# Kernel optimization log

Hardware: AMD Instinct MI355X
Metric: run time of the kernel (lower is better)

Reference implementation:

```python
import jax, jax.numpy as jnp
import numpy as np

D_MODEL = 1024  # scale uses sqrt(d_model), matching the source's sqrt(C)

def setup_inputs() -> dict:
    key = jax.random.key(0)
    kx, kq, kk, kv = jax.random.split(key, 4)
    B, T, C, H = 8, 2048, D_MODEL, 64
    s = 1.0 / np.sqrt(C)
    return {
        "x": jax.random.normal(kx, (B, T, C), dtype=jnp.float32),
        "Wq": jax.random.normal(kq, (C, H), dtype=jnp.float32) * s,
        "Wk": jax.random.normal(kk, (C, H), dtype=jnp.float32) * s,
        "Wv": jax.random.normal(kv, (C, H), dtype=jnp.float32) * s,
    }

def reference(x, Wq, Wk, Wv):
    B, T, C = x.shape
    q = jnp.einsum("btc,ch->bth", x, Wq)
    k = jnp.einsum("btc,ch->bth", x, Wk)
    v = jnp.einsum("btc,ch->bth", x, Wv)
    # scores scaled by 1/sqrt(C) (C = d_model), faithful to source
    wei = jnp.einsum("bth,bsh->bts", q, k) / jnp.sqrt(jnp.float32(C))
    causal = jnp.tril(jnp.ones((T, T), dtype=bool))  # [T, T]
    wei = jnp.where(causal, wei, -jnp.inf)
    wei = jax.nn.softmax(wei, axis=-1)
    out = jnp.einsum("bts,bsh->bth", wei, v)
    return out
```

## Files before the change

kernel.cpp:

```cpp
#include <hip/hip_runtime.h>

typedef unsigned short u16;
typedef __attribute__((ext_vector_type(4))) float f32x4;
typedef __attribute__((ext_vector_type(8))) short bf16x8;
typedef __attribute__((ext_vector_type(4))) u16 u16x4;
typedef __attribute__((ext_vector_type(8))) u16 u16x8;

#define MFMA(a, b, c) __builtin_amdgcn_mfma_f32_16x16x32_bf16(a, b, c, 0, 0, 0)

__device__ __forceinline__ u16 f2bf(float f) {
    unsigned u = __float_as_uint(f);
    u += 0x7fffu + ((u >> 16) & 1u);
    return (u16)(u >> 16);
}
__device__ __forceinline__ float bf2f(u16 h) {
    unsigned u = ((unsigned)h) << 16;
    return __uint_as_float(u);
}

__device__ __forceinline__ void load_lds16(const void* g, void* l) {
    __builtin_amdgcn_global_load_lds((const __attribute__((address_space(1))) void*)g,
                                     (__attribute__((address_space(3))) void*)l,
                                     16, 0, 0);
}

__global__ void wt_pack(const float* __restrict__ Wq, const float* __restrict__ Wk,
                        const float* __restrict__ Wv, u16* __restrict__ Wtt) {
    const int k = blockIdx.x;
    const int n = threadIdx.x;
    const float* W = (n < 64) ? Wq : (n < 128 ? Wk : Wv);
    const float v = W[(size_t)k * 64 + (n & 63)];
    const int kt = k >> 5, ks = k & 31, c = ks >> 3, ci = ks & 7;
    Wtt[(size_t)kt * 6144 + n * 32 + (((c ^ (n & 3)) << 3) + ci)] = f2bf(v);
}

__global__ __launch_bounds__(256, 4) void qkv_gemm(const float* __restrict__ x,
                                                   const u16* __restrict__ Wtt,
                                                   u16* __restrict__ qo,
                                                   u16* __restrict__ ko,
                                                   u16* __restrict__ vT) {
    const int tid = threadIdx.x;
    const int lane = tid & 63, wave = tid >> 6;
    const int lr = lane & 15, lg = lane >> 4;
    const int m0 = blockIdx.x * 32;

    __shared__ __align__(16) float xs[2][32 * 32];
    __shared__ __align__(16) u16 ws[2][192 * 32];

    f32x4 acc[2][3];
#pragma unroll
    for (int m = 0; m < 2; ++m)
#pragma unroll
        for (int n = 0; n < 3; ++n) acc[m][n] = (f32x4){0.f, 0.f, 0.f, 0.f};

    const int xrow = tid >> 3, xc = tid & 7;

#define QSTAGE(bufi, kt_)                                                              \
    {                                                                                  \
        load_lds16(x + (size_t)(m0 + xrow) * 1024 + (kt_)*32 + ((xc ^ (xrow & 7)) << 2), \
                   &xs[bufi][wave * 256]);                                             \
        _Pragma("unroll") for (int j = 0; j < 3; ++j) {                                \
            load_lds16(Wtt + (size_t)(kt_)*6144 + (j * 256 + tid) * 8,                 \
                       &ws[bufi][(j * 256 + wave * 64) * 8]);                          \
        }                                                                              \
    }

    QSTAGE(0, 0);
    __syncthreads();

    for (int kt = 0; kt < 32; ++kt) {
        const int cur = kt & 1;
        if (kt < 31) QSTAGE(cur ^ 1, kt + 1);

        bf16x8 a[2];
#pragma unroll
        for (int mm = 0; mm < 2; ++mm) {
            const int rr = mm * 16 + lr;
            const int g0 = lg * 2;
            f32x4 f0 = *(const f32x4*)&xs[cur][rr * 32 + ((g0 ^ (rr & 7)) << 2)];
            f32x4 f1 = *(const f32x4*)&xs[cur][rr * 32 + (((g0 + 1) ^ (rr & 7)) << 2)];
            bf16x8 t;
#pragma unroll
            for (int i = 0; i < 4; ++i) {
                t[i] = (short)f2bf(f0[i]);
                t[i + 4] = (short)f2bf(f1[i]);
            }
            a[mm] = t;
        }
#pragma unroll
        for (int nl = 0; nl < 3; ++nl) {
            const int row = (wave * 3 + nl) * 16 + lr;
            const bf16x8 b = *(const bf16x8*)&ws[cur][row * 32 + ((lg ^ (row & 3)) << 3)];
            acc[0][nl] = MFMA(a[0], b, acc[0][nl]);
            acc[1][nl] = MFMA(a[1], b, acc[1][nl]);
        }
        __syncthreads();
    }

    const float SCQ = 0.0450842200277801f;
    const int bb = m0 >> 11;
    const int tb = m0 & 2047;
#pragma unroll
    for (int mm = 0; mm < 2; ++mm)
#pragma unroll
        for (int nl = 0; nl < 3; ++nl) {
            const int col = (wave * 3 + nl) * 16 + lr;
            const int rl = mm * 16 + lg * 4;
            if (col < 64) {
#pragma unroll
                for (int r = 0; r < 4; ++r)
                    qo[(size_t)(m0 + rl + r) * 64 + col] = f2bf(acc[mm][nl][r] * SCQ);
            } else if (col < 128) {
#pragma unroll
                for (int r = 0; r < 4; ++r)
                    ko[(size_t)(m0 + rl + r) * 64 + (col - 64)] = f2bf(acc[mm][nl][r]);
            } else {
                u16x4 pk;
#pragma unroll
                for (int r = 0; r < 4; ++r) pk[r] = f2bf(acc[mm][nl][r]);
                *(u16x4*)&vT[(size_t)(bb * 64 + (col - 128)) * 2048 + tb + rl] = pk;
            }
        }
}

#define PPITCH 72
__global__ __launch_bounds__(256, 3) void attn_part(const u16* __restrict__ q,
                                                    const u16* __restrict__ k,
                                                    const u16* __restrict__ vT,
                                                    u16* __restrict__ Opb,
                                                    float* __restrict__ Lp) {
    const int b = blockIdx.x & 7;
    int g = blockIdx.x >> 3;
    int qt = 31, rem = g;
    while (rem >= (qt >> 3) + 1) { rem -= (qt >> 3) + 1; --qt; }
    const int c0 = rem;
    const int q0 = qt * 64;
    const int kv_lo = c0 * 512;
    const int kv_hi = min(kv_lo + 512, q0 + 64);
    const int ntiles = (kv_hi - kv_lo) >> 6;
    const int slot = (b * 32 + qt) * 4 + c0;

    __shared__ __align__(16) u16 lK[2][64 * 64];
    __shared__ __align__(16) u16 lV[2][64 * 64];
    __shared__ __align__(16) u16 lP[4][16 * PPITCH];

    const int tid = threadIdx.x;
    const int wave = tid >> 6, lane = tid & 63;
    const int lr = lane & 15, lg = lane >> 4;

    const u16* qb = q + (size_t)b * 2048 * 64;
    const u16* kb = k + (size_t)b * 2048 * 64;
    const u16* vb = vT + (size_t)b * 64 * 2048;

    const int myrow = q0 + wave * 16 + lr;
    const bf16x8 qf0 = *(const bf16x8*)(qb + (size_t)myrow * 64 + lg * 8);
    const bf16x8 qf1 = *(const bf16x8*)(qb + (size_t)myrow * 64 + 32 + lg * 8);

    f32x4 oacc[4];
#pragma unroll
    for (int n = 0; n < 4; ++n) oacc[n] = (f32x4){0.f, 0.f, 0.f, 0.f};
    float rs = 0.f;

#define ASTAGE(bufi, kv0_)                                                             \
    {                                                                                  \
        _Pragma("unroll") for (int j = 0; j < 2; ++j) {                                \
            const int cid = j * 256 + wave * 64 + lane;                                \
            const int row = cid >> 3, cc = cid & 7;                                    \
            load_lds16(kb + (size_t)((kv0_) + row) * 64 + ((cc ^ (row & 7)) << 3),     \
                       &lK[bufi][(j * 256 + wave * 64) * 8]);                          \
            load_lds16(vb + (size_t)row * 2048 + (kv0_) + ((cc ^ (row & 7)) << 3),     \
                       &lV[bufi][(j * 256 + wave * 64) * 8]);                          \
        }                                                                              \
    }

    ASTAGE(0, kv_lo);
    __syncthreads();

    for (int it = 0; it < ntiles; ++it) {
        const int cur = it & 1;
        if (it + 1 < ntiles) ASTAGE(cur ^ 1, kv_lo + (it + 1) * 64);

        const int kv0 = kv_lo + it * 64;
        if (kv0 <= q0 + wave * 16 + 15) {
            f32x4 s[4];
            __builtin_amdgcn_s_setprio(1);
#pragma unroll
            for (int n = 0; n < 4; ++n) {
                const int row = n * 16 + lr;
                const bf16x8 kf0 = *(const bf16x8*)&lK[cur][row * 64 + ((lg ^ (row & 7)) << 3)];
                const bf16x8 kf1 =
                    *(const bf16x8*)&lK[cur][row * 64 + (((4 + lg) ^ (row & 7)) << 3)];
                f32x4 a = (f32x4){0.f, 0.f, 0.f, 0.f};
                a = MFMA(kf0, qf0, a);
                a = MFMA(kf1, qf1, a);
                s[n] = a;
            }
            __builtin_amdgcn_s_setprio(0);

            const bool msk = (kv0 + 63 > q0 + wave * 16);
#pragma unroll
            for (int n = 0; n < 4; ++n) {
                u16x4 pk;
#pragma unroll
                for (int r = 0; r < 4; ++r) {
                    const int kvi = kv0 + n * 16 + lg * 4 + r;
                    const float p = (!msk || kvi <= myrow) ? exp2f(s[n][r]) : 0.f;
                    rs += p;
                    pk[r] = f2bf(p);
                }
                *(u16x4*)&lP[wave][lr * PPITCH + n * 16 + lg * 4] = pk;
            }

            __builtin_amdgcn_s_setprio(1);
#pragma unroll
            for (int kc = 0; kc < 2; ++kc) {
                const bf16x8 pf = *(const bf16x8*)&lP[wave][lr * PPITCH + kc * 32 + lg * 8];
#pragma unroll
                for (int n = 0; n < 4; ++n) {
                    const int row = n * 16 + lr;
                    const bf16x8 vf =
                        *(const bf16x8*)&lV[cur][row * 64 + (((kc * 4 + lg) ^ (row & 7)) << 3)];
                    oacc[n] = MFMA(pf, vf, oacc[n]);
                }
            }
            __builtin_amdgcn_s_setprio(0);
        }
        __syncthreads();
    }

    rs += __shfl_xor(rs, 16);
    rs += __shfl_xor(rs, 32);
    if (lane < 16) Lp[slot * 64 + wave * 16 + lr] = rs;

    u16* op = Opb + (size_t)slot * 4096 + wave * 1024;
#pragma unroll
    for (int n = 0; n < 4; ++n)
#pragma unroll
        for (int r = 0; r < 4; ++r)
            op[n * 256 + (lg * 4 + r) * 16 + lr] = f2bf(oacc[n][r]);
}

__global__ __launch_bounds__(256) void attn_combine(const u16* __restrict__ Opb,
                                                    const float* __restrict__ Lp,
                                                    float* __restrict__ out) {
    const int gid = blockIdx.x * 256 + threadIdx.x;
    const int colg = gid & 7;
    const int row = gid >> 3;
    const int b = row >> 11, tt = row & 2047;
    const int qt = tt >> 6, i = tt & 63;
    const int nc = (qt >> 3) + 1;
    const size_t sbase = (size_t)(b * 32 + qt) * 4;
    const int sub0 = (i >> 4) * 1024 + (colg >> 1) * 256 + (i & 15) * 16 + (colg & 1) * 8;

    float O[8] = {0.f, 0.f, 0.f, 0.f, 0.f, 0.f, 0.f, 0.f};
    float L = 0.f;
    for (int c = 0; c < nc; ++c) {
        const u16x8 v = *(const u16x8*)&Opb[(sbase + c) * 4096 + sub0];
#pragma unroll
        for (int j = 0; j < 8; ++j) O[j] += bf2f(v[j]);
        L += Lp[(sbase + c) * 64 + i];
    }
    const float rinv = 1.0f / L;
    f32x4 o0, o1;
#pragma unroll
    for (int j = 0; j < 4; ++j) {
        o0[j] = O[j] * rinv;
        o1[j] = O[4 + j] * rinv;
    }
    float* ob = out + (size_t)row * 64 + colg * 8;
    *(f32x4*)(ob) = o0;
    *(f32x4*)(ob + 4) = o1;
}

extern "C" void kernel_launch(void* const* d_in, const int* in_sizes, int n_in,
                              void* d_out, int out_size, void* d_ws, size_t ws_size,
                              hipStream_t stream) {
    const float* x = (const float*)d_in[0];
    const float* Wq = (const float*)d_in[1];
    const float* Wk = (const float*)d_in[2];
    const float* Wv = (const float*)d_in[3];
    float* out = (float*)d_out;

    char* ws = (char*)d_ws;
    u16* Wtt = (u16*)ws;
    u16* qb = (u16*)(ws + (512 << 10));
    u16* kb = (u16*)(ws + (512 << 10) + (2 << 20));
    u16* vT = (u16*)(ws + (512 << 10) + (4 << 20));
    u16* Opb = (u16*)(ws + (8 << 20));
    float* Lp = (float*)(ws + (20 << 20));

    wt_pack<<<1024, 192, 0, stream>>>(Wq, Wk, Wv, Wtt);
    qkv_gemm<<<512, 256, 0, stream>>>(x, Wtt, qb, kb, vT);
    attn_part<<<640, 256, 0, stream>>>(qb, kb, vT, Opb, Lp);
    attn_combine<<<512, 256, 0, stream>>>(Opb, Lp, out);
}
```

Measured before the change: 56.28 us.

## Retile QKV projection GEMM to 64x64 tiles split per matrix

The QKV projection GEMM moves from 32-row tiles covering all 192 output columns to 64-row by 64-column tiles, one matrix (Q, K or V) per block. The grid grows from 512 to 768 blocks, the K-step doubles to 64 so there are fewer loop iterations and barriers, and the weight packing layout and swizzle are rebuilt to match. Each block now reads 64 rows of fp32 x per stage but covers only one of three outputs, so x is read from global memory three times instead of once. The larger LDS footprint lowers the launch-bounds occupancy hint from 4 to 3.

```diff
diff --git a/kernel.cpp b/kernel.cpp
--- a/kernel.cpp
+++ b/kernel.cpp
@@ -30,11 +30,12 @@
     const int n = threadIdx.x;
     const float* W = (n < 64) ? Wq : (n < 128 ? Wk : Wv);
     const float v = W[(size_t)k * 64 + (n & 63)];
-    const int kt = k >> 5, ks = k & 31, c = ks >> 3, ci = ks & 7;
-    Wtt[(size_t)kt * 6144 + n * 32 + (((c ^ (n & 3)) << 3) + ci)] = f2bf(v);
-}
-
-__global__ __launch_bounds__(256, 4) void qkv_gemm(const float* __restrict__ x,
+    const int mat = n >> 6, nl = n & 63;
+    const int kt = k >> 6, ks = k & 63, c = ks >> 3, ci = ks & 7;
+    Wtt[(size_t)((mat * 16 + kt) * 64 + nl) * 64 + (((c ^ (nl & 7)) << 3) + ci)] = f2bf(v);
+}
+
+__global__ __launch_bounds__(256, 3) void qkv_gemm(const float* __restrict__ x,
                                                    const u16* __restrict__ Wtt,
                                                    u16* __restrict__ qo,
                                                    u16* __restrict__ ko,
@@ -42,85 +43,91 @@
     const int tid = threadIdx.x;
     const int lane = tid & 63, wave = tid >> 6;
     const int lr = lane & 15, lg = lane >> 4;
-    const int m0 = blockIdx.x * 32;
-
-    __shared__ __align__(16) float xs[2][32 * 32];
-    __shared__ __align__(16) u16 ws[2][192 * 32];
-
-    f32x4 acc[2][3];
-#pragma unroll
-    for (int m = 0; m < 2; ++m)
-#pragma unroll
-        for (int n = 0; n < 3; ++n) acc[m][n] = (f32x4){0.f, 0.f, 0.f, 0.f};
-
-    const int xrow = tid >> 3, xc = tid & 7;
-
-#define QSTAGE(bufi, kt_)                                                              \
-    {                                                                                  \
-        load_lds16(x + (size_t)(m0 + xrow) * 1024 + (kt_)*32 + ((xc ^ (xrow & 7)) << 2), \
-                   &xs[bufi][wave * 256]);                                             \
-        _Pragma("unroll") for (int j = 0; j < 3; ++j) {                                \
-            load_lds16(Wtt + (size_t)(kt_)*6144 + (j * 256 + tid) * 8,                 \
-                       &ws[bufi][(j * 256 + wave * 64) * 8]);                          \
-        }                                                                              \
+    const int mat = blockIdx.x >> 8;
+    const int m0 = (blockIdx.x & 255) * 64;
+
+    __shared__ __align__(16) float xs[2][64 * 64];
+    __shared__ __align__(16) u16 ws[2][64 * 64];
+
+    f32x4 acc[4];
+#pragma unroll
+    for (int m = 0; m < 4; ++m) acc[m] = (f32x4){0.f, 0.f, 0.f, 0.f};
+
+#define QSTAGE(bufi, kt_)                                                               \
+    {                                                                                   \
+        _Pragma("unroll") for (int j = 0; j < 4; ++j) {                                 \
+            const int cid = j * 256 + tid;                                              \
+            const int row = cid >> 4, cc = cid & 15;                                    \
+            load_lds16(x + (size_t)(m0 + row) * 1024 + (kt_)*64 +                       \
+                           ((cc ^ (row & 7)) << 2),                                     \
+                       &xs[bufi][(j * 256 + wave * 64) * 4]);                           \
+        }                                                                               \
+        _Pragma("unroll") for (int j = 0; j < 2; ++j) {                                 \
+            const int cid = j * 256 + tid;                                              \
+            load_lds16(Wtt + (size_t)(mat * 16 + (kt_)) * 4096 + cid * 8,               \
+                       &ws[bufi][(j * 256 + wave * 64) * 8]);                           \
+        }                                                                               \
     }
 
     QSTAGE(0, 0);
     __syncthreads();
 
-    for (int kt = 0; kt < 32; ++kt) {
+    for (int kt = 0; kt < 16; ++kt) {
         const int cur = kt & 1;
-        if (kt < 31) QSTAGE(cur ^ 1, kt + 1);
-
-        bf16x8 a[2];
-#pragma unroll
-        for (int mm = 0; mm < 2; ++mm) {
-            const int rr = mm * 16 + lr;
-            const int g0 = lg * 2;
-            f32x4 f0 = *(const f32x4*)&xs[cur][rr * 32 + ((g0 ^ (rr & 7)) << 2)];
-            f32x4 f1 = *(const f32x4*)&xs[cur][rr * 32 + (((g0 + 1) ^ (rr & 7)) << 2)];
-            bf16x8 t;
-#pragma unroll
-            for (int i = 0; i < 4; ++i) {
-                t[i] = (short)f2bf(f0[i]);
-                t[i + 4] = (short)f2bf(f1[i]);
+        if (kt < 15) QSTAGE(cur ^ 1, kt + 1);
+
+#pragma unroll
+        for (int h = 0; h < 2; ++h) {
+            const int wrow = wave * 16 + lr;
+            const int cb = h * 4 + lg;
+            const bf16x8 b = *(const bf16x8*)&ws[cur][wrow * 64 + ((cb ^ (wrow & 7)) << 3)];
+#pragma unroll
+            for (int mm = 0; mm < 4; ++mm) {
+                const int rr = mm * 16 + lr;
+                const int c0 = h * 8 + lg * 2;
+                f32x4 f0 = *(const f32x4*)&xs[cur][rr * 64 + ((c0 ^ (rr & 7)) << 2)];
+                f32x4 f1 = *(const f32x4*)&xs[cur][rr * 64 + (((c0 + 1) ^ (rr & 7)) << 2)];
+                bf16x8 a;
+#pragma unroll
+                for (int i = 0; i < 4; ++i) {
+                    a[i] = (short)f2bf(f0[i]);
+                    a[i + 4] = (short)f2bf(f1[i]);
+                }
+                acc[mm] = MFMA(a, b, acc[mm]);
             }
-            a[mm] = t;
-        }
-#pragma unroll
-        for (int nl = 0; nl < 3; ++nl) {
-            const int row = (wave * 3 + nl) * 16 + lr;
-            const bf16x8 b = *(const bf16x8*)&ws[cur][row * 32 + ((lg ^ (row & 3)) << 3)];
-            acc[0][nl] = MFMA(a[0], b, acc[0][nl]);
-            acc[1][nl] = MFMA(a[1], b, acc[1][nl]);
         }
         __syncthreads();
     }
 
     const float SCQ = 0.0450842200277801f;
-    const int bb = m0 >> 11;
-    const int tb = m0 & 2047;
-#pragma unroll
-    for (int mm = 0; mm < 2; ++mm)
-#pragma unroll
-        for (int nl = 0; nl < 3; ++nl) {
-            const int col = (wave * 3 + nl) * 16 + lr;
-            const int rl = mm * 16 + lg * 4;
-            if (col < 64) {
-#pragma unroll
-                for (int r = 0; r < 4; ++r)
-                    qo[(size_t)(m0 + rl + r) * 64 + col] = f2bf(acc[mm][nl][r] * SCQ);
-            } else if (col < 128) {
-#pragma unroll
-                for (int r = 0; r < 4; ++r)
-                    ko[(size_t)(m0 + rl + r) * 64 + (col - 64)] = f2bf(acc[mm][nl][r]);
-            } else {
-                u16x4 pk;
-#pragma unroll
-                for (int r = 0; r < 4; ++r) pk[r] = f2bf(acc[mm][nl][r]);
-                *(u16x4*)&vT[(size_t)(bb * 64 + (col - 128)) * 2048 + tb + rl] = pk;
-            }
-        }
+    const int col = wave * 16 + lr;
+    if (mat == 0) {
+#pragma unroll
+        for (int mm = 0; mm < 4; ++mm) {
+            const int rl = m0 + mm * 16 + lg * 4;
+#pragma unroll
+            for (int r = 0; r < 4; ++r)
+                qo[(size_t)(rl + r) * 64 + col] = f2bf(acc[mm][r] * SCQ);
+        }
+    } else if (mat == 1) {
+#pragma unroll
+        for (int mm = 0; mm < 4; ++mm) {
+            const int rl = m0 + mm * 16 + lg * 4;
+#pragma unroll
+            for (int r = 0; r < 4; ++r)
+                ko[(size_t)(rl + r) * 64 + col] = f2bf(acc[mm][r]);
+        }
+    } else {
+        const int bb = m0 >> 11;
+        const int tb = m0 & 2047;
+#pragma unroll
+        for (int mm = 0; mm < 4; ++mm) {
+            u16x4 pk;
+#pragma unroll
+            for (int r = 0; r < 4; ++r) pk[r] = f2bf(acc[mm][r]);
+            *(u16x4*)&vT[(size_t)(bb * 64 + col) * 2048 + tb + mm * 16 + lg * 4] = pk;
+        }
+    }
 }
 
 #define PPITCH 72
@@ -290,7 +297,7 @@
     float* Lp = (float*)(ws + (20 << 20));
 
     wt_pack<<<1024, 192, 0, stream>>>(Wq, Wk, Wv, Wtt);
-    qkv_gemm<<<512, 256, 0, stream>>>(x, Wtt, qb, kb, vT);
+    qkv_gemm<<<768, 256, 0, stream>>>(x, Wtt, qb, kb, vT);
     attn_part<<<640, 256, 0, stream>>>(qb, kb, vT, Opb, Lp);
     attn_combine<<<512, 256, 0, stream>>>(Opb, Lp, out);
 }
```

Result: slower. 60.42 us (+7.4%).

## Retile QKV projection GEMM to 64x96 block tiles with 2x2 wave grid

Applied to the files above, without the earlier changes.

Each QKV projection block now computes a 64-row by 96-column tile instead of 32 rows by all 192 columns. The K step grows from 32 to 64, and the four waves are arranged as a 2x2 grid. The weight pack layout changes to match: column-tile-major with an 8-way XOR swizzle. The aim is more MFMA work per LDS stage and fewer loop iterations and barriers. In exchange, each x row is now loaded and converted to bf16 by two blocks, and the larger LDS footprint lowers occupancy to two blocks per CU.

```diff
diff --git a/kernel.cpp b/kernel.cpp
--- a/kernel.cpp
+++ b/kernel.cpp
@@ -30,11 +30,12 @@
     const int n = threadIdx.x;
     const float* W = (n < 64) ? Wq : (n < 128 ? Wk : Wv);
     const float v = W[(size_t)k * 64 + (n & 63)];
-    const int kt = k >> 5, ks = k & 31, c = ks >> 3, ci = ks & 7;
-    Wtt[(size_t)kt * 6144 + n * 32 + (((c ^ (n & 3)) << 3) + ci)] = f2bf(v);
-}
-
-__global__ __launch_bounds__(256, 4) void qkv_gemm(const float* __restrict__ x,
+    const int nt = n / 96, nl = n % 96;
+    const int kt = k >> 6, ks = k & 63, c = ks >> 3, ci = ks & 7;
+    Wtt[(size_t)((nt * 16 + kt) * 96 + nl) * 64 + (((c ^ (nl & 7)) << 3) + ci)] = f2bf(v);
+}
+
+__global__ __launch_bounds__(256, 2) void qkv_gemm(const float* __restrict__ x,
                                                    const u16* __restrict__ Wtt,
                                                    u16* __restrict__ qo,
                                                    u16* __restrict__ ko,
@@ -42,10 +43,12 @@
     const int tid = threadIdx.x;
     const int lane = tid & 63, wave = tid >> 6;
     const int lr = lane & 15, lg = lane >> 4;
-    const int m0 = blockIdx.x * 32;
-
-    __shared__ __align__(16) float xs[2][32 * 32];
-    __shared__ __align__(16) u16 ws[2][192 * 32];
+    const int wr = wave >> 1, wc = wave & 1;
+    const int mt = blockIdx.x >> 1, nt = blockIdx.x & 1;
+    const int m0 = mt * 64;
+
+    __shared__ __align__(16) float xs[2][64 * 64];
+    __shared__ __align__(16) u16 ws[2][96 * 64];
 
     f32x4 acc[2][3];
 #pragma unroll
@@ -53,46 +56,54 @@
 #pragma unroll
         for (int n = 0; n < 3; ++n) acc[m][n] = (f32x4){0.f, 0.f, 0.f, 0.f};
 
-    const int xrow = tid >> 3, xc = tid & 7;
-
-#define QSTAGE(bufi, kt_)                                                              \
-    {                                                                                  \
-        load_lds16(x + (size_t)(m0 + xrow) * 1024 + (kt_)*32 + ((xc ^ (xrow & 7)) << 2), \
-                   &xs[bufi][wave * 256]);                                             \
-        _Pragma("unroll") for (int j = 0; j < 3; ++j) {                                \
-            load_lds16(Wtt + (size_t)(kt_)*6144 + (j * 256 + tid) * 8,                 \
-                       &ws[bufi][(j * 256 + wave * 64) * 8]);                          \
-        }                                                                              \
+#define QSTAGE(bufi, kt_)                                                               \
+    {                                                                                   \
+        _Pragma("unroll") for (int j = 0; j < 4; ++j) {                                 \
+            const int cid = j * 256 + tid;                                              \
+            const int row = cid >> 4, cc = cid & 15;                                    \
+            load_lds16(x + (size_t)(m0 + row) * 1024 + (kt_)*64 +                       \
+                           ((cc ^ (row & 7)) << 2),                                     \
+                       &xs[bufi][(j * 256 + wave * 64) * 4]);                           \
+        }                                                                               \
+        _Pragma("unroll") for (int j = 0; j < 3; ++j) {                                 \
+            const int cid = j * 256 + tid;                                              \
+            load_lds16(Wtt + (size_t)((nt * 16 + (kt_)) * 96) * 64 + cid * 8,           \
+                       &ws[bufi][(j * 256 + wave * 64) * 8]);                           \
+        }                                                                               \
     }
 
     QSTAGE(0, 0);
     __syncthreads();
 
-    for (int kt = 0; kt < 32; ++kt) {
+    for (int kt = 0; kt < 16; ++kt) {
         const int cur = kt & 1;
-        if (kt < 31) QSTAGE(cur ^ 1, kt + 1);
-
-        bf16x8 a[2];
-#pragma unroll
-        for (int mm = 0; mm < 2; ++mm) {
-            const int rr = mm * 16 + lr;
-            const int g0 = lg * 2;
-            f32x4 f0 = *(const f32x4*)&xs[cur][rr * 32 + ((g0 ^ (rr & 7)) << 2)];
-            f32x4 f1 = *(const f32x4*)&xs[cur][rr * 32 + (((g0 + 1) ^ (rr & 7)) << 2)];
-            bf16x8 t;
-#pragma unroll
-            for (int i = 0; i < 4; ++i) {
-                t[i] = (short)f2bf(f0[i]);
-                t[i + 4] = (short)f2bf(f1[i]);
-            }
-            a[mm] = t;
-        }
-#pragma unroll
-        for (int nl = 0; nl < 3; ++nl) {
-            const int row = (wave * 3 + nl) * 16 + lr;
-            const bf16x8 b = *(const bf16x8*)&ws[cur][row * 32 + ((lg ^ (row & 3)) << 3)];
-            acc[0][nl] = MFMA(a[0], b, acc[0][nl]);
-            acc[1][nl] = MFMA(a[1], b, acc[1][nl]);
+        if (kt < 15) QSTAGE(cur ^ 1, kt + 1);
+
+#pragma unroll
+        for (int h = 0; h < 2; ++h) {
+            bf16x8 a[2];
+#pragma unroll
+            for (int mm = 0; mm < 2; ++mm) {
+                const int rr = wr * 32 + mm * 16 + lr;
+                const int c0 = h * 8 + lg * 2;
+                f32x4 f0 = *(const f32x4*)&xs[cur][rr * 64 + ((c0 ^ (rr & 7)) << 2)];
+                f32x4 f1 = *(const f32x4*)&xs[cur][rr * 64 + (((c0 + 1) ^ (rr & 7)) << 2)];
+                bf16x8 t;
+#pragma unroll
+                for (int i = 0; i < 4; ++i) {
+                    t[i] = (short)f2bf(f0[i]);
+                    t[i + 4] = (short)f2bf(f1[i]);
+                }
+                a[mm] = t;
+            }
+#pragma unroll
+            for (int nl = 0; nl < 3; ++nl) {
+                const int row = wc * 48 + nl * 16 + lr;
+                const int cb = h * 4 + lg;
+                const bf16x8 b = *(const bf16x8*)&ws[cur][row * 64 + ((cb ^ (row & 7)) << 3)];
+                acc[0][nl] = MFMA(a[0], b, acc[0][nl]);
+                acc[1][nl] = MFMA(a[1], b, acc[1][nl]);
+            }
         }
         __syncthreads();
     }
@@ -104,8 +115,8 @@
     for (int mm = 0; mm < 2; ++mm)
 #pragma unroll
         for (int nl = 0; nl < 3; ++nl) {
-            const int col = (wave * 3 + nl) * 16 + lr;
-            const int rl = mm * 16 + lg * 4;
+            const int col = nt * 96 + wc * 48 + nl * 16 + lr;
+            const int rl = wr * 32 + mm * 16 + lg * 4;
             if (col < 64) {
 #pragma unroll
                 for (int r = 0; r < 4; ++r)
```

New measurement: 58.05 us. +3.1%, slower.

## Split QKV projection along K with LDS-resident weights and a combine pass

Applied to the files above, without the earlier changes.

The QKV GEMM is restructured so each block owns one of 8 K-chunks of 128. That block keeps the whole 192x128 bf16 weight slice resident in LDS and streams 256 rows of x through a double buffer, instead of reloading weights on every K step. Each block writes bf16 partial sums to a large workspace buffer, and a new qkv_combine kernel sums the 8 partials and applies the Q scale. It also writes q, k and the transposed v. This cuts repeated weight loads and LDS restaging, but adds a large partial-sum write and read through global memory and an extra launch. Rounding the partials to bf16 before summing also loses some accuracy.

```diff
diff --git a/kernel.cpp b/kernel.cpp
--- a/kernel.cpp
+++ b/kernel.cpp
@@ -30,97 +30,134 @@
     const int n = threadIdx.x;
     const float* W = (n < 64) ? Wq : (n < 128 ? Wk : Wv);
     const float v = W[(size_t)k * 64 + (n & 63)];
-    const int kt = k >> 5, ks = k & 31, c = ks >> 3, ci = ks & 7;
-    Wtt[(size_t)kt * 6144 + n * 32 + (((c ^ (n & 3)) << 3) + ci)] = f2bf(v);
-}
-
-__global__ __launch_bounds__(256, 4) void qkv_gemm(const float* __restrict__ x,
+    const int kc = k >> 7, kl = k & 127, c = kl >> 3, ci = kl & 7;
+    const int cs = (c & 8) | ((c & 7) ^ (n & 7));
+    Wtt[((size_t)(kc * 192 + n) * 16 + cs) * 8 + ci] = f2bf(v);
+}
+
+__global__ __launch_bounds__(256, 2) void qkv_gemm(const float* __restrict__ x,
                                                    const u16* __restrict__ Wtt,
+                                                   u16* __restrict__ Pp) {
+    const int tid = threadIdx.x;
+    const int lane = tid & 63, wave = tid >> 6;
+    const int lr = lane & 15, lg = lane >> 4;
+    const int wc = wave;
+    const int kc = blockIdx.x & 7;
+    const int mb = blockIdx.x >> 3;
+
+    __shared__ __align__(16) u16 wsm[192 * 128];
+    __shared__ __align__(16) float xs[2][32 * 128];
+
+#pragma unroll
+    for (int j = 0; j < 12; ++j) {
+        const int cid = j * 256 + tid;
+        load_lds16(Wtt + (size_t)kc * 24576 + cid * 8, &wsm[(j * 256 + wave * 64) * 8]);
+    }
+
+#define XSTAGE(bufi, mrow_)                                                            \
+    {                                                                                  \
+        _Pragma("unroll") for (int j = 0; j < 4; ++j) {                                \
+            const int cid = j * 256 + tid;                                             \
+            const int row = cid >> 5, cch = cid & 31;                                  \
+            const int csw = (cch & 0x18) | ((cch & 7) ^ (row & 7));                    \
+            load_lds16(x + (size_t)((mrow_) + row) * 1024 + kc * 128 + (csw << 2),     \
+                       &xs[bufi][(j * 256 + wave * 64) * 4]);                          \
+        }                                                                              \
+    }
+
+    XSTAGE(0, mb * 256);
+    __syncthreads();
+
+    for (int mi = 0; mi < 8; ++mi) {
+        const int cur = mi & 1;
+        if (mi < 7) XSTAGE(cur ^ 1, mb * 256 + (mi + 1) * 32);
+
+        f32x4 acc[2][3];
+#pragma unroll
+        for (int m = 0; m < 2; ++m)
+#pragma unroll
+            for (int n = 0; n < 3; ++n) acc[m][n] = (f32x4){0.f, 0.f, 0.f, 0.f};
+
+#pragma unroll
+        for (int ks = 0; ks < 4; ++ks) {
+            bf16x8 a[2];
+#pragma unroll
+            for (int mm = 0; mm < 2; ++mm) {
+                const int rr = mm * 16 + lr;
+                const int c0 = ks * 8 + lg * 2;
+                const int cs0 = (ks * 8) | ((lg * 2) ^ (rr & 7));
+                const int cs1 = (ks * 8) | ((lg * 2 + 1) ^ (rr & 7));
+                (void)c0;
+                f32x4 f0 = *(const f32x4*)&xs[cur][rr * 128 + cs0 * 4];
+                f32x4 f1 = *(const f32x4*)&xs[cur][rr * 128 + cs1 * 4];
+                bf16x8 t;
+#pragma unroll
+                for (int i = 0; i < 4; ++i) {
+                    t[i] = (short)f2bf(f0[i]);
+                    t[i + 4] = (short)f2bf(f1[i]);
+                }
+                a[mm] = t;
+            }
+#pragma unroll
+            for (int nl = 0; nl < 3; ++nl) {
+                const int row = wc * 48 + nl * 16 + lr;
+                const int cb = ks * 4 + lg;
+                const int cs = (cb & 8) | ((cb & 7) ^ (row & 7));
+                const bf16x8 b = *(const bf16x8*)&wsm[row * 128 + cs * 8];
+                acc[0][nl] = MFMA(a[0], b, acc[0][nl]);
+                acc[1][nl] = MFMA(a[1], b, acc[1][nl]);
+            }
+        }
+
+        const int mrow = mb * 256 + mi * 32;
+        u16* pp = Pp + (size_t)kc * 3145728;
+#pragma unroll
+        for (int mm = 0; mm < 2; ++mm)
+#pragma unroll
+            for (int nl = 0; nl < 3; ++nl) {
+                const int col = wc * 48 + nl * 16 + lr;
+#pragma unroll
+                for (int r = 0; r < 4; ++r)
+                    pp[(size_t)(mrow + mm * 16 + lg * 4 + r) * 192 + col] =
+                        f2bf(acc[mm][nl][r]);
+            }
+        __syncthreads();
+    }
+}
+
+__global__ __launch_bounds__(256) void qkv_combine(const u16* __restrict__ Pp,
                                                    u16* __restrict__ qo,
                                                    u16* __restrict__ ko,
                                                    u16* __restrict__ vT) {
-    const int tid = threadIdx.x;
-    const int lane = tid & 63, wave = tid >> 6;
-    const int lr = lane & 15, lg = lane >> 4;
-    const int m0 = blockIdx.x * 32;
-
-    __shared__ __align__(16) float xs[2][32 * 32];
-    __shared__ __align__(16) u16 ws[2][192 * 32];
-
-    f32x4 acc[2][3];
-#pragma unroll
-    for (int m = 0; m < 2; ++m)
-#pragma unroll
-        for (int n = 0; n < 3; ++n) acc[m][n] = (f32x4){0.f, 0.f, 0.f, 0.f};
-
-    const int xrow = tid >> 3, xc = tid & 7;
-
-#define QSTAGE(bufi, kt_)                                                              \
-    {                                                                                  \
-        load_lds16(x + (size_t)(m0 + xrow) * 1024 + (kt_)*32 + ((xc ^ (xrow & 7)) << 2), \
-                   &xs[bufi][wave * 256]);                                             \
-        _Pragma("unroll") for (int j = 0; j < 3; ++j) {                                \
-            load_lds16(Wtt + (size_t)(kt_)*6144 + (j * 256 + tid) * 8,                 \
-                       &ws[bufi][(j * 256 + wave * 64) * 8]);                          \
-        }                                                                              \
-    }
-
-    QSTAGE(0, 0);
-    __syncthreads();
-
-    for (int kt = 0; kt < 32; ++kt) {
-        const int cur = kt & 1;
-        if (kt < 31) QSTAGE(cur ^ 1, kt + 1);
-
-        bf16x8 a[2];
-#pragma unroll
-        for (int mm = 0; mm < 2; ++mm) {
-            const int rr = mm * 16 + lr;
-            const int g0 = lg * 2;
-            f32x4 f0 = *(const f32x4*)&xs[cur][rr * 32 + ((g0 ^ (rr & 7)) << 2)];
-            f32x4 f1 = *(const f32x4*)&xs[cur][rr * 32 + (((g0 + 1) ^ (rr & 7)) << 2)];
-            bf16x8 t;
-#pragma unroll
-            for (int i = 0; i < 4; ++i) {
-                t[i] = (short)f2bf(f0[i]);
-                t[i + 4] = (short)f2bf(f1[i]);
-            }
-            a[mm] = t;
-        }
-#pragma unroll
-        for (int nl = 0; nl < 3; ++nl) {
-            const int row = (wave * 3 + nl) * 16 + lr;
-            const bf16x8 b = *(const bf16x8*)&ws[cur][row * 32 + ((lg ^ (row & 3)) << 3)];
-            acc[0][nl] = MFMA(a[0], b, acc[0][nl]);
-            acc[1][nl] = MFMA(a[1], b, acc[1][nl]);
-        }
-        __syncthreads();
+    const int gid = blockIdx.x * 256 + threadIdx.x;
+    const int row = gid / 24;
+    const int col0 = (gid % 24) * 8;
+
+    float O[8] = {0.f, 0.f, 0.f, 0.f, 0.f, 0.f, 0.f, 0.f};
+#pragma unroll
+    for (int kc = 0; kc < 8; ++kc) {
+        const u16x8 v = *(const u16x8*)&Pp[(size_t)kc * 3145728 + (size_t)row * 192 + col0];
+#pragma unroll
+        for (int j = 0; j < 8; ++j) O[j] += bf2f(v[j]);
     }
 
     const float SCQ = 0.0450842200277801f;
-    const int bb = m0 >> 11;
-    const int tb = m0 & 2047;
-#pragma unroll
-    for (int mm = 0; mm < 2; ++mm)
-#pragma unroll
-        for (int nl = 0; nl < 3; ++nl) {
-            const int col = (wave * 3 + nl) * 16 + lr;
-            const int rl = mm * 16 + lg * 4;
-            if (col < 64) {
-#pragma unroll
-                for (int r = 0; r < 4; ++r)
-                    qo[(size_t)(m0 + rl + r) * 64 + col] = f2bf(acc[mm][nl][r] * SCQ);
-            } else if (col < 128) {
-#pragma unroll
-                for (int r = 0; r < 4; ++r)
-                    ko[(size_t)(m0 + rl + r) * 64 + (col - 64)] = f2bf(acc[mm][nl][r]);
-            } else {
-                u16x4 pk;
-#pragma unroll
-                for (int r = 0; r < 4; ++r) pk[r] = f2bf(acc[mm][nl][r]);
-                *(u16x4*)&vT[(size_t)(bb * 64 + (col - 128)) * 2048 + tb + rl] = pk;
-            }
-        }
+    if (col0 < 64) {
+        u16x8 pk;
+#pragma unroll
+        for (int j = 0; j < 8; ++j) pk[j] = f2bf(O[j] * SCQ);
+        *(u16x8*)&qo[(size_t)row * 64 + col0] = pk;
+    } else if (col0 < 128) {
+        u16x8 pk;
+#pragma unroll
+        for (int j = 0; j < 8; ++j) pk[j] = f2bf(O[j]);
+        *(u16x8*)&ko[(size_t)row * 64 + (col0 - 64)] = pk;
+    } else {
+        const int bb = row >> 11, t = row & 2047;
+#pragma unroll
+        for (int j = 0; j < 8; ++j)
+            vT[(size_t)(bb * 64 + col0 - 128 + j) * 2048 + t] = f2bf(O[j]);
+    }
 }
 
 #define PPITCH 72
@@ -286,11 +323,13 @@
     u16* qb = (u16*)(ws + (512 << 10));
     u16* kb = (u16*)(ws + (512 << 10) + (2 << 20));
     u16* vT = (u16*)(ws + (512 << 10) + (4 << 20));
-    u16* Opb = (u16*)(ws + (8 << 20));
+    u16* Pp = (u16*)(ws + ((13 << 20) >> 1));
+    u16* Opb = (u16*)(ws + ((13 << 20) >> 1));
     float* Lp = (float*)(ws + (20 << 20));
 
     wt_pack<<<1024, 192, 0, stream>>>(Wq, Wk, Wv, Wtt);
-    qkv_gemm<<<512, 256, 0, stream>>>(x, Wtt, qb, kb, vT);
+    qkv_gemm<<<512, 256, 0, stream>>>(x, Wtt, Pp);
+    qkv_combine<<<1536, 256, 0, stream>>>(Pp, qb, kb, vT);
     attn_part<<<640, 256, 0, stream>>>(qb, kb, vT, Opb, Lp);
     attn_combine<<<512, 256, 0, stream>>>(Opb, Lp, out);
 }
```

Result: slower. 65.85 us (+17.0%).
